# Kernel tuning notes

Measured on AMD Instinct MI355X. Metric: run time of the kernel, lower is better.

## Reference

```python
import jax, jax.numpy as jnp
import numpy as np

N_REF, N_IN, D_FEAT, P, N_ELEM = 4096, 8192, 512, 256, 4


def setup_inputs() -> dict:
    key = jax.random.key(0)
    k1, k2, k3, k4, k5 = jax.random.split(key, 5)
    return {
        "Alpha": jax.random.normal(k1, (P, N_REF), dtype=jnp.float32) * 0.05,
        "X_ref": jax.random.normal(k2, (N_REF, D_FEAT), dtype=jnp.float32),
        "desc": jax.random.normal(k3, (N_IN, D_FEAT), dtype=jnp.float32),
        "Z_ref": jax.random.randint(k4, (N_REF,), 0, N_ELEM, dtype=jnp.int32),
        "Z": jax.random.randint(k5, (N_IN,), 0, N_ELEM, dtype=jnp.int32),
        "expK": 2,
    }


def reference(Alpha, X_ref, desc, Z_ref, Z, expK):
    # Per-element grouped kernel: K[i, j] = (X_ref[i] . desc[j])**expK,
    # contribution only where ref atom i and query atom j share the element.
    # This is exactly the gather -> per-element GEMM+pow -> combine -> scatter
    # of the original module, expressed as one masked dense computation.
    K = jnp.power(jnp.matmul(X_ref, desc.T), expK)          # [N_ref, N_in]
    same_elem = Z_ref[:, None] == Z[None, :]                # [N_ref, N_in]
    K_masked = jnp.where(same_elem, K, jnp.zeros((), K.dtype))
    y = jnp.matmul(Alpha, K_masked)                          # [P, N_in]
    return y
```

## Files before the change

kernel.cpp:

```cpp
#include <hip/hip_runtime.h>
#include <stdint.h>

#define P_DIM 256
#define NREF  4096
#define NIN   8192
#define DF    512

typedef __bf16 bf16x8 __attribute__((ext_vector_type(8)));
typedef float  f32x4  __attribute__((ext_vector_type(4)));

static __device__ __forceinline__ unsigned short f2bf(float f) {
    uint32_t u = __builtin_bit_cast(uint32_t, f);
    u += 0x7FFFu + ((u >> 16) & 1u);
    return (unsigned short)(u >> 16);
}
static __device__ __forceinline__ float bf2f(unsigned short u) {
    return __builtin_bit_cast(float, (uint32_t)u << 16);
}

__global__ void cast3(const float* __restrict__ s0, unsigned short* __restrict__ d0, int n0,
                      const float* __restrict__ s1, unsigned short* __restrict__ d1, int n1,
                      const float* __restrict__ s2, unsigned short* __restrict__ d2, int n2) {
    int total = n0 + n1 + n2;
    int stride = gridDim.x * blockDim.x;
    for (int i = blockIdx.x * blockDim.x + threadIdx.x; i < total; i += stride) {
        const float4* s; ushort4* d; int j = i;
        if (j < n0) { s = (const float4*)s0; d = (ushort4*)d0; }
        else if ((j -= n0) < n1) { s = (const float4*)s1; d = (ushort4*)d1; }
        else { j -= n1; s = (const float4*)s2; d = (ushort4*)d2; }
        float4 v = s[j];
        ushort4 o;
        o.x = f2bf(v.x); o.y = f2bf(v.y); o.z = f2bf(v.z); o.w = f2bf(v.w);
        d[j] = o;
    }
}

__global__ void reduce3(float* __restrict__ out, const unsigned short* __restrict__ parts,
                        int n4, size_t partElems) {
    int i = blockIdx.x * blockDim.x + threadIdx.x;
    if (i >= n4) return;
    float4 a = ((const float4*)out)[i];
    const ushort4* p0 = (const ushort4*)(parts);
    const ushort4* p1 = (const ushort4*)(parts + partElems);
    const ushort4* p2 = (const ushort4*)(parts + 2 * partElems);
    ushort4 u0 = p0[i], u1 = p1[i], u2 = p2[i];
    a.x += bf2f(u0.x) + bf2f(u1.x) + bf2f(u2.x);
    a.y += bf2f(u0.y) + bf2f(u1.y) + bf2f(u2.y);
    a.z += bf2f(u0.z) + bf2f(u1.z) + bf2f(u2.z);
    a.w += bf2f(u0.w) + bf2f(u1.w) + bf2f(u2.w);
    ((float4*)out)[i] = a;
}

template <int BM, int BN, int WAVES, int WR, int WC, bool SQMASK>
static __device__ __forceinline__ void gemm_body(
    const unsigned short* __restrict__ A,
    const unsigned short* __restrict__ B,
    void* __restrict__ C0,
    void* __restrict__ C1,
    const int* __restrict__ ZA,
    const int* __restrict__ ZB,
    int M, int N, int KC)
{
    constexpr int BK = 64;
    constexpr int RT = BM / WR / 16;
    constexpr int CT = BN / WC / 16;
    __shared__ unsigned short tA[BM * BK];
    __shared__ unsigned short tB[BN * BK];

    const int tid  = threadIdx.x;
    const int wave = tid >> 6;
    const int lane = tid & 63;
    const int wr = wave / WC, wc = wave % WC;
    const int m0 = blockIdx.y * BM, n0 = blockIdx.x * BN;
    const int waveM = wr * (BM / WR), waveN = wc * (BN / WC);
    const int lrow = lane >> 3, ls = lane & 7;
    const int l15 = lane & 15, lq = lane >> 4;
    const size_t Kd = (size_t)KC * gridDim.z;
    const int kbeg = blockIdx.z * KC;

    f32x4 acc[RT][CT];
#pragma unroll
    for (int r = 0; r < RT; ++r)
#pragma unroll
        for (int c = 0; c < CT; ++c)
            acc[r][c] = (f32x4){0.f, 0.f, 0.f, 0.f};

    constexpr int TOTAL_CB = (BM + BN) / 8;
    constexpr int CB_PER_WAVE = TOTAL_CB / WAVES;
    static_assert(TOTAL_CB % WAVES == 0, "staging split");

    for (int k0 = kbeg; k0 < kbeg + KC; k0 += BK) {
        __syncthreads();
#pragma unroll
        for (int it = 0; it < CB_PER_WAVE; ++it) {
            int cb = wave + it * WAVES;
            bool isB = (cb >= BM / 8);
            int cb2 = isB ? cb - BM / 8 : cb;
            int row = cb2 * 8 + lrow;
            int g = ls ^ (row & 7);
            const unsigned short* gp = (isB ? B : A)
                + (size_t)((isB ? n0 : m0) + row) * Kd + (size_t)(k0 + g * 8);
            unsigned short* lp = (isB ? tB : tA) + cb2 * (8 * BK);
            __builtin_amdgcn_global_load_lds(
                (const __attribute__((address_space(1))) void*)gp,
                (__attribute__((address_space(3))) void*)lp,
                16, 0, 0);
        }
        __syncthreads();
#pragma unroll
        for (int kk = 0; kk < BK; kk += 32) {
            const int cbase = kk >> 3;
            bf16x8 af[RT], bfr[CT];
#pragma unroll
            for (int r = 0; r < RT; ++r) {
                int m = waveM + r * 16 + l15;
                int ch = (cbase + lq) ^ (m & 7);
                af[r] = *(const bf16x8*)&tA[m * BK + ch * 8];
            }
#pragma unroll
            for (int c = 0; c < CT; ++c) {
                int n = waveN + c * 16 + l15;
                int ch = (cbase + lq) ^ (n & 7);
                bfr[c] = *(const bf16x8*)&tB[n * BK + ch * 8];
            }
#pragma unroll
            for (int r = 0; r < RT; ++r)
#pragma unroll
                for (int c = 0; c < CT; ++c)
                    acc[r][c] = __builtin_amdgcn_mfma_f32_16x16x32_bf16(
                        af[r], bfr[c], acc[r][c], 0, 0, 0);
        }
    }

    int nIdx[CT];
    int zb[CT];
#pragma unroll
    for (int c = 0; c < CT; ++c) {
        nIdx[c] = n0 + waveN + c * 16 + l15;
        if (SQMASK) zb[c] = ZB[nIdx[c]];
    }
    const bool toPart = (!SQMASK) && (blockIdx.z != 0);
    unsigned short* partBase = (unsigned short*)C1
        + (size_t)(blockIdx.z ? blockIdx.z - 1 : 0) * (size_t)M * (size_t)N;
#pragma unroll
    for (int r = 0; r < RT; ++r) {
        int mbase = m0 + waveM + r * 16 + lq * 4;
#pragma unroll
        for (int reg = 0; reg < 4; ++reg) {
            int m = mbase + reg;
            size_t rowoff = (size_t)m * (size_t)N;
            if (SQMASK) {
                int za = ZA[m];
                unsigned short* outp = (unsigned short*)C0;
#pragma unroll
                for (int c = 0; c < CT; ++c) {
                    float v = acc[r][c][reg];
                    float kv = (za == zb[c]) ? v * v : 0.0f;
                    outp[rowoff + nIdx[c]] = f2bf(kv);
                }
            } else if (!toPart) {
                float* outp = (float*)C0;
#pragma unroll
                for (int c = 0; c < CT; ++c)
                    outp[rowoff + nIdx[c]] = acc[r][c][reg];
            } else {
#pragma unroll
                for (int c = 0; c < CT; ++c)
                    partBase[rowoff + nIdx[c]] = f2bf(acc[r][c][reg]);
            }
        }
    }
}

__global__ __launch_bounds__(256) void g1_desc_xref(
    const unsigned short* __restrict__ A, const unsigned short* __restrict__ B,
    void* __restrict__ C0, const int* __restrict__ ZA, const int* __restrict__ ZB,
    int M, int N, int KC) {
    gemm_body<128, 128, 4, 2, 2, true>(A, B, C0, nullptr, ZA, ZB, M, N, KC);
}

__global__ __launch_bounds__(256) void g2_alpha_kt(
    const unsigned short* __restrict__ A, const unsigned short* __restrict__ B,
    void* __restrict__ C0, void* __restrict__ C1,
    int M, int N, int KC) {
    gemm_body<128, 128, 4, 2, 2, false>(A, B, C0, C1, nullptr, nullptr, M, N, KC);
}

extern "C" void kernel_launch(void* const* d_in, const int* in_sizes, int n_in,
                              void* d_out, int out_size, void* d_ws, size_t ws_size,
                              hipStream_t stream) {
    const float* Alpha = (const float*)d_in[0];
    const float* X_ref = (const float*)d_in[1];
    const float* desc  = (const float*)d_in[2];
    const int*   Z_ref = (const int*)d_in[3];
    const int*   Z     = (const int*)d_in[4];
    float* out = (float*)d_out;

    unsigned short* Xb = (unsigned short*)d_ws;
    unsigned short* Db = Xb + (size_t)NREF * DF;
    unsigned short* Ab = Db + (size_t)NIN * DF;
    unsigned short* Kt = Ab + (size_t)P_DIM * NREF;
    unsigned short* part = (unsigned short*)d_ws;

    cast3<<<4096, 256, 0, stream>>>(
        X_ref, Xb, NREF * DF / 4,
        desc,  Db, NIN * DF / 4,
        Alpha, Ab, P_DIM * NREF / 4);

    dim3 g1(NREF / 128, NIN / 128, 1);
    g1_desc_xref<<<g1, 256, 0, stream>>>(
        Db, Xb, (void*)Kt, Z, Z_ref, NIN, NREF, DF);

    dim3 g2(NIN / 128, P_DIM / 128, 4);
    g2_alpha_kt<<<g2, 256, 0, stream>>>(
        Ab, Kt, (void*)out, (void*)part, P_DIM, NIN, NREF / 4);

    reduce3<<<(P_DIM * NIN / 4 + 255) / 256, 256, 0, stream>>>(
        out, part, P_DIM * NIN / 4, (size_t)P_DIM * NIN);
}
```

Before: 164.6 us.

## Fuse kernel-matrix GEMM and Alpha GEMM into one kernel keeping K tile in LDS

Replaces the two-GEMM pipeline, which wrote the masked squared kernel matrix K to global memory and read it back, with one fused kernel. Each block computes a 64x128 tile of K, masks and squares it into LDS as bf16, then multiplies the Alpha rows directly against it into a 256x64 accumulator, iterating over a quarter of the reference atoms. This removes the 64 MB K round trip through HBM. In exchange, each block streams Alpha from global memory without LDS staging, the grid drops to 512 blocks, and it carries a large per-thread accumulator that may limit occupancy.

```diff
diff --git a/kernel.cpp b/kernel.cpp
--- a/kernel.cpp
+++ b/kernel.cpp
@@ -5,6 +5,11 @@
 #define NREF  4096
 #define NIN   8192
 #define DF    512
+
+#define BJ     64
+#define TI     128
+#define ISPLIT 4
+#define IR     (NREF / ISPLIT)
 
 typedef __bf16 bf16x8 __attribute__((ext_vector_type(8)));
 typedef float  f32x4  __attribute__((ext_vector_type(4)));
@@ -51,139 +56,165 @@
     ((float4*)out)[i] = a;
 }
 
-template <int BM, int BN, int WAVES, int WR, int WC, bool SQMASK>
-static __device__ __forceinline__ void gemm_body(
-    const unsigned short* __restrict__ A,
-    const unsigned short* __restrict__ B,
-    void* __restrict__ C0,
-    void* __restrict__ C1,
-    const int* __restrict__ ZA,
-    const int* __restrict__ ZB,
-    int M, int N, int KC)
+__global__ __launch_bounds__(256) void fused_y(
+    const unsigned short* __restrict__ Db,
+    const unsigned short* __restrict__ Xb,
+    const unsigned short* __restrict__ Ab,
+    const int* __restrict__ Z,
+    const int* __restrict__ Zr,
+    float* __restrict__ outp,
+    unsigned short* __restrict__ part)
 {
     constexpr int BK = 64;
-    constexpr int RT = BM / WR / 16;
-    constexpr int CT = BN / WC / 16;
-    __shared__ unsigned short tA[BM * BK];
-    __shared__ unsigned short tB[BN * BK];
+    __shared__ unsigned short tA[BJ * BK];
+    __shared__ unsigned short tB[TI * BK];
+    __shared__ unsigned short Tl[BJ * TI];
 
     const int tid  = threadIdx.x;
     const int wave = tid >> 6;
     const int lane = tid & 63;
-    const int wr = wave / WC, wc = wave % WC;
-    const int m0 = blockIdx.y * BM, n0 = blockIdx.x * BN;
-    const int waveM = wr * (BM / WR), waveN = wc * (BN / WC);
+    const int l15  = lane & 15, lq = lane >> 4;
     const int lrow = lane >> 3, ls = lane & 7;
-    const int l15 = lane & 15, lq = lane >> 4;
-    const size_t Kd = (size_t)KC * gridDim.z;
-    const int kbeg = blockIdx.z * KC;
-
-    f32x4 acc[RT][CT];
-#pragma unroll
-    for (int r = 0; r < RT; ++r)
-#pragma unroll
-        for (int c = 0; c < CT; ++c)
-            acc[r][c] = (f32x4){0.f, 0.f, 0.f, 0.f};
-
-    constexpr int TOTAL_CB = (BM + BN) / 8;
-    constexpr int CB_PER_WAVE = TOTAL_CB / WAVES;
-    static_assert(TOTAL_CB % WAVES == 0, "staging split");
-
-    for (int k0 = kbeg; k0 < kbeg + KC; k0 += BK) {
+    const int j0    = blockIdx.x * BJ;
+    const int ibase = blockIdx.y * IR;
+
+    const int waMa = (wave >> 1) * 32;
+    const int waNa = (wave & 1) * 64;
+    const int waPb = wave * 64;
+
+    int zaj[2][4];
+#pragma unroll
+    for (int r = 0; r < 2; ++r)
+#pragma unroll
+        for (int reg = 0; reg < 4; ++reg)
+            zaj[r][reg] = Z[j0 + waMa + r * 16 + lq * 4 + reg];
+
+    f32x4 accY[4][4];
+#pragma unroll
+    for (int r = 0; r < 4; ++r)
+#pragma unroll
+        for (int c = 0; c < 4; ++c)
+            accY[r][c] = (f32x4){0.f, 0.f, 0.f, 0.f};
+
+#pragma unroll 1
+    for (int it = 0; it < IR / TI; ++it) {
+        const int i1 = ibase + it * TI;
+
+        f32x4 accT[2][4];
+#pragma unroll
+        for (int r = 0; r < 2; ++r)
+#pragma unroll
+            for (int c = 0; c < 4; ++c)
+                accT[r][c] = (f32x4){0.f, 0.f, 0.f, 0.f};
+
+#pragma unroll 1
+        for (int k0 = 0; k0 < DF; k0 += BK) {
+            __syncthreads();
+#pragma unroll
+            for (int itc = 0; itc < 6; ++itc) {
+                int cb = wave + itc * 4;
+                bool isB = cb >= (BJ / 8);
+                int cb2 = isB ? cb - BJ / 8 : cb;
+                int row = cb2 * 8 + lrow;
+                int g = ls ^ (row & 7);
+                const unsigned short* gp = isB
+                    ? Xb + (size_t)(i1 + row) * DF + (size_t)(k0 + g * 8)
+                    : Db + (size_t)(j0 + row) * DF + (size_t)(k0 + g * 8);
+                unsigned short* lp = (isB ? tB : tA) + cb2 * (8 * BK);
+                __builtin_amdgcn_global_load_lds(
+                    (const __attribute__((address_space(1))) void*)gp,
+                    (__attribute__((address_space(3))) void*)lp,
+                    16, 0, 0);
+            }
+            __syncthreads();
+#pragma unroll
+            for (int kk = 0; kk < BK; kk += 32) {
+                const int cbase = kk >> 3;
+                bf16x8 af[2], bfv[4];
+#pragma unroll
+                for (int r = 0; r < 2; ++r) {
+                    int m = waMa + r * 16 + l15;
+                    int ch = (cbase + lq) ^ (m & 7);
+                    af[r] = *(const bf16x8*)&tA[m * BK + ch * 8];
+                }
+#pragma unroll
+                for (int c = 0; c < 4; ++c) {
+                    int n = waNa + c * 16 + l15;
+                    int ch = (cbase + lq) ^ (n & 7);
+                    bfv[c] = *(const bf16x8*)&tB[n * BK + ch * 8];
+                }
+#pragma unroll
+                for (int r = 0; r < 2; ++r)
+#pragma unroll
+                    for (int c = 0; c < 4; ++c)
+                        accT[r][c] = __builtin_amdgcn_mfma_f32_16x16x32_bf16(
+                            af[r], bfv[c], accT[r][c], 0, 0, 0);
+            }
+        }
+
+        int zbv[4];
+#pragma unroll
+        for (int c = 0; c < 4; ++c)
+            zbv[c] = Zr[i1 + waNa + c * 16 + l15];
+#pragma unroll
+        for (int r = 0; r < 2; ++r)
+#pragma unroll
+            for (int reg = 0; reg < 4; ++reg) {
+                int j = waMa + r * 16 + lq * 4 + reg;
+                int za = zaj[r][reg];
+#pragma unroll
+                for (int c = 0; c < 4; ++c) {
+                    int i = waNa + c * 16 + l15;
+                    float v = accT[r][c][reg];
+                    float kv = (za == zbv[c]) ? v * v : 0.0f;
+                    Tl[j * TI + (((i >> 3) ^ (j & 15)) << 3) + (i & 7)] = f2bf(kv);
+                }
+            }
         __syncthreads();
-#pragma unroll
-        for (int it = 0; it < CB_PER_WAVE; ++it) {
-            int cb = wave + it * WAVES;
-            bool isB = (cb >= BM / 8);
-            int cb2 = isB ? cb - BM / 8 : cb;
-            int row = cb2 * 8 + lrow;
-            int g = ls ^ (row & 7);
-            const unsigned short* gp = (isB ? B : A)
-                + (size_t)((isB ? n0 : m0) + row) * Kd + (size_t)(k0 + g * 8);
-            unsigned short* lp = (isB ? tB : tA) + cb2 * (8 * BK);
-            __builtin_amdgcn_global_load_lds(
-                (const __attribute__((address_space(1))) void*)gp,
-                (__attribute__((address_space(3))) void*)lp,
-                16, 0, 0);
-        }
-        __syncthreads();
-#pragma unroll
-        for (int kk = 0; kk < BK; kk += 32) {
-            const int cbase = kk >> 3;
-            bf16x8 af[RT], bfr[CT];
-#pragma unroll
-            for (int r = 0; r < RT; ++r) {
-                int m = waveM + r * 16 + l15;
-                int ch = (cbase + lq) ^ (m & 7);
-                af[r] = *(const bf16x8*)&tA[m * BK + ch * 8];
-            }
-#pragma unroll
-            for (int c = 0; c < CT; ++c) {
-                int n = waveN + c * 16 + l15;
-                int ch = (cbase + lq) ^ (n & 7);
-                bfr[c] = *(const bf16x8*)&tB[n * BK + ch * 8];
-            }
-#pragma unroll
-            for (int r = 0; r < RT; ++r)
-#pragma unroll
-                for (int c = 0; c < CT; ++c)
-                    acc[r][c] = __builtin_amdgcn_mfma_f32_16x16x32_bf16(
-                        af[r], bfr[c], acc[r][c], 0, 0, 0);
+
+#pragma unroll
+        for (int ks = 0; ks < TI; ks += 32) {
+            bf16x8 afa[4], bfb[4];
+#pragma unroll
+            for (int rt = 0; rt < 4; ++rt) {
+                int p = waPb + rt * 16 + l15;
+                size_t gi = (size_t)p * NREF + (size_t)(i1 + ks + lq * 8);
+                afa[rt] = *(const bf16x8*)&Ab[gi];
+            }
+#pragma unroll
+            for (int ct = 0; ct < 4; ++ct) {
+                int j = ct * 16 + l15;
+                int c8 = (ks >> 3) + lq;
+                int slot = c8 ^ (j & 15);
+                bfb[ct] = *(const bf16x8*)&Tl[j * TI + slot * 8];
+            }
+#pragma unroll
+            for (int rt = 0; rt < 4; ++rt)
+#pragma unroll
+                for (int ct = 0; ct < 4; ++ct)
+                    accY[rt][ct] = __builtin_amdgcn_mfma_f32_16x16x32_bf16(
+                        afa[rt], bfb[ct], accY[rt][ct], 0, 0, 0);
         }
     }
 
-    int nIdx[CT];
-    int zb[CT];
-#pragma unroll
-    for (int c = 0; c < CT; ++c) {
-        nIdx[c] = n0 + waveN + c * 16 + l15;
-        if (SQMASK) zb[c] = ZB[nIdx[c]];
-    }
-    const bool toPart = (!SQMASK) && (blockIdx.z != 0);
-    unsigned short* partBase = (unsigned short*)C1
-        + (size_t)(blockIdx.z ? blockIdx.z - 1 : 0) * (size_t)M * (size_t)N;
-#pragma unroll
-    for (int r = 0; r < RT; ++r) {
-        int mbase = m0 + waveM + r * 16 + lq * 4;
+    const int z = blockIdx.y;
+#pragma unroll
+    for (int rt = 0; rt < 4; ++rt) {
 #pragma unroll
         for (int reg = 0; reg < 4; ++reg) {
-            int m = mbase + reg;
-            size_t rowoff = (size_t)m * (size_t)N;
-            if (SQMASK) {
-                int za = ZA[m];
-                unsigned short* outp = (unsigned short*)C0;
-#pragma unroll
-                for (int c = 0; c < CT; ++c) {
-                    float v = acc[r][c][reg];
-                    float kv = (za == zb[c]) ? v * v : 0.0f;
-                    outp[rowoff + nIdx[c]] = f2bf(kv);
-                }
-            } else if (!toPart) {
-                float* outp = (float*)C0;
-#pragma unroll
-                for (int c = 0; c < CT; ++c)
-                    outp[rowoff + nIdx[c]] = acc[r][c][reg];
-            } else {
-#pragma unroll
-                for (int c = 0; c < CT; ++c)
-                    partBase[rowoff + nIdx[c]] = f2bf(acc[r][c][reg]);
+            int p = waPb + rt * 16 + lq * 4 + reg;
+#pragma unroll
+            for (int ct = 0; ct < 4; ++ct) {
+                int jg = j0 + ct * 16 + l15;
+                float v = accY[rt][ct][reg];
+                if (z == 0) {
+                    outp[(size_t)p * NIN + jg] = v;
+                } else {
+                    part[(size_t)(z - 1) * P_DIM * NIN + (size_t)p * NIN + jg] = f2bf(v);
+                }
             }
         }
     }
-}
-
-__global__ __launch_bounds__(256) void g1_desc_xref(
-    const unsigned short* __restrict__ A, const unsigned short* __restrict__ B,
-    void* __restrict__ C0, const int* __restrict__ ZA, const int* __restrict__ ZB,
-    int M, int N, int KC) {
-    gemm_body<128, 128, 4, 2, 2, true>(A, B, C0, nullptr, ZA, ZB, M, N, KC);
-}
-
-__global__ __launch_bounds__(256) void g2_alpha_kt(
-    const unsigned short* __restrict__ A, const unsigned short* __restrict__ B,
-    void* __restrict__ C0, void* __restrict__ C1,
-    int M, int N, int KC) {
-    gemm_body<128, 128, 4, 2, 2, false>(A, B, C0, C1, nullptr, nullptr, M, N, KC);
 }
 
 extern "C" void kernel_launch(void* const* d_in, const int* in_sizes, int n_in,
@@ -196,24 +227,18 @@
     const int*   Z     = (const int*)d_in[4];
     float* out = (float*)d_out;
 
-    unsigned short* Xb = (unsigned short*)d_ws;
-    unsigned short* Db = Xb + (size_t)NREF * DF;
-    unsigned short* Ab = Db + (size_t)NIN * DF;
-    unsigned short* Kt = Ab + (size_t)P_DIM * NREF;
-    unsigned short* part = (unsigned short*)d_ws;
+    unsigned short* Xb   = (unsigned short*)d_ws;
+    unsigned short* Db   = Xb + (size_t)NREF * DF;
+    unsigned short* Ab   = Db + (size_t)NIN * DF;
+    unsigned short* part = Ab + (size_t)P_DIM * NREF;
 
     cast3<<<4096, 256, 0, stream>>>(
         X_ref, Xb, NREF * DF / 4,
         desc,  Db, NIN * DF / 4,
         Alpha, Ab, P_DIM * NREF / 4);
 
-    dim3 g1(NREF / 128, NIN / 128, 1);
-    g1_desc_xref<<<g1, 256, 0, stream>>>(
-        Db, Xb, (void*)Kt, Z, Z_ref, NIN, NREF, DF);
-
-    dim3 g2(NIN / 128, P_DIM / 128, 4);
-    g2_alpha_kt<<<g2, 256, 0, stream>>>(
-        Ab, Kt, (void*)out, (void*)part, P_DIM, NIN, NREF / 4);
+    dim3 gf(NIN / BJ, ISPLIT);
+    fused_y<<<gf, 256, 0, stream>>>(Db, Xb, Ab, Z, Z_ref, out, part);
 
     reduce3<<<(P_DIM * NIN / 4 + 255) / 256, 256, 0, stream>>>(
         out, part, P_DIM * NIN / 4, (size_t)P_DIM * NIN);
```

Measured after the change: 252.9 us. 53.6% more time.
